# Performance work log

Measured on AMD Instinct MI355X. Metric: run time of the kernel, lower is better.

## Reference

```python
import jax, jax.numpy as jnp
import numpy as np

HEAD_SIZE = 64
N_EMBED = 1024
B, T = 8, 2048


def setup_inputs() -> dict:
    key = jax.random.key(0)
    ks = jax.random.split(key, 7)
    s = lambda fan_in: 1.0 / np.sqrt(fan_in)
    return {
        "x": jax.random.normal(ks[0], (B, T, N_EMBED), dtype=jnp.float32),
        # Linear weights stored as (in, out) so projection is x @ W + b
        "Wk": jax.random.uniform(ks[1], (N_EMBED, HEAD_SIZE), jnp.float32, -s(N_EMBED), s(N_EMBED)),
        "bk": jax.random.uniform(ks[2], (HEAD_SIZE,), jnp.float32, -s(N_EMBED), s(N_EMBED)),
        "Wq": jax.random.uniform(ks[3], (N_EMBED, HEAD_SIZE), jnp.float32, -s(N_EMBED), s(N_EMBED)),
        "bq": jax.random.uniform(ks[4], (HEAD_SIZE,), jnp.float32, -s(N_EMBED), s(N_EMBED)),
        "Wv": jax.random.uniform(ks[5], (N_EMBED, HEAD_SIZE), jnp.float32, -s(N_EMBED), s(N_EMBED)),
        "bv": jax.random.uniform(ks[6], (HEAD_SIZE,), jnp.float32, -s(N_EMBED), s(N_EMBED)),
    }


def reference(x, Wk, bk, Wq, bq, Wv, bv):
    Bb, Tt, C = x.shape
    k = x @ Wk + bk  # [B,T,H]
    q = x @ Wq + bq
    v = x @ Wv + bv
    # NOTE: original computes k @ q^T (keys as rows, queries as cols)
    wei = jnp.einsum("bth,bsh->bts", k, q) * (C ** -0.5)  # [B,T,T]
    causal = jnp.tril(jnp.ones((Tt, Tt), dtype=bool))
    wei = jnp.where(causal, wei, -jnp.inf)
    # softplus instead of softmax; softplus(-inf) = 0, stable via logaddexp
    wei = jnp.logaddexp(wei, 0.0)
    # dropout omitted (eval mode / deterministic reference)
    out = jnp.einsum("bts,bsh->bth", wei, v)  # [B,T,H]
    return out
```

## Files before the change

### kernel.cpp

```cpp
#include <hip/hip_runtime.h>
#include <hip/hip_bf16.h>
#include <stdint.h>

#define HEAD 64
#define CEMB 1024
#define BB 8
#define TSEQ 2048

typedef __attribute__((ext_vector_type(8))) short bf16x8;
typedef __attribute__((ext_vector_type(4))) float f32x4;

__device__ __forceinline__ unsigned short f2bf(float f) {
    union { float f; uint32_t u; } c; c.f = f;
    uint32_t u = c.u + 0x7FFF + ((c.u >> 16) & 1);
    return (unsigned short)(u >> 16);
}
__device__ __forceinline__ ushort4 f4bf(float4 v) {
    ushort4 u; u.x = f2bf(v.x); u.y = f2bf(v.y); u.z = f2bf(v.z); u.w = f2bf(v.w);
    return u;
}

__global__ __launch_bounds__(256) void prep_w(
        const float* __restrict__ Wk, const float* __restrict__ bk,
        const float* __restrict__ Wq, const float* __restrict__ bq,
        const float* __restrict__ Wv, const float* __restrict__ bv,
        unsigned short* __restrict__ WTf, float* __restrict__ biasb) {
    __shared__ float Wl[3][32][64];
    const int kc = blockIdx.x;
    const int tid = threadIdx.x;
    const float* Ws[3] = {Wk, Wq, Wv};
    const int row = tid >> 3, cf = (tid & 7) * 8;
    #pragma unroll
    for (int p = 0; p < 3; p++) {
        const float* W = Ws[p] + (long)(kc * 32 + row) * 64 + cf;
        float4 v0 = *(const float4*)(W);
        float4 v1 = *(const float4*)(W + 4);
        *(float4*)(&Wl[p][row][cf]) = v0;
        *(float4*)(&Wl[p][row][cf + 4]) = v1;
    }
    __syncthreads();
    #pragma unroll
    for (int i = 0; i < 3; i++) {
        int cid = i * 256 + tid;
        int lane = cid & 63;
        int l15 = lane & 15, q4 = lane >> 4;
        int n = (cid >> 6) * 16 + l15;
        int p = n >> 6, col = n & 63;
        float scale = (p == 1) ? 0.03125f : 1.0f;
        unsigned short o[8];
        for (int e = 0; e < 8; e++) o[e] = f2bf(Wl[p][q4 * 8 + e][col] * scale);
        *(int4*)(WTf + (long)kc * 6144 + (long)cid * 8) = *(int4*)o;
    }
    if (kc == 0 && tid < 192) {
        const float* bs[3] = {bk, bq, bv};
        int p = tid >> 6;
        biasb[tid] = bs[p][tid & 63] * ((p == 1) ? 0.03125f : 1.0f);
    }
}

__global__ __launch_bounds__(256) void proj_gemm(
        const float* __restrict__ x, const unsigned short* __restrict__ WTf,
        const float* __restrict__ biasb,
        unsigned short* __restrict__ Kb, unsigned short* __restrict__ Qb,
        unsigned short* __restrict__ VTb) {
    __shared__ __align__(16) unsigned short As[32 * 1032];

    const int tid = threadIdx.x;
    const int lane = tid & 63, w = tid >> 6;
    const int l15 = lane & 15, q4 = lane >> 4;
    const int mw = w & 1, nw = w >> 1;
    const long rowbase = (long)blockIdx.x * 32;

    {
        const int r = tid >> 3, c0 = (tid & 7) * 4;
        const float* xr = x + (rowbase + r) * CEMB + c0;
        float4 buf[32];
        #pragma unroll
        for (int i = 0; i < 32; i++) buf[i] = *(const float4*)(xr + i * 32);
        unsigned short* lr = As + r * 1032 + c0;
        #pragma unroll
        for (int i = 0; i < 32; i++) *(ushort4*)(lr + i * 32) = f4bf(buf[i]);
    }
    __syncthreads();

    f32x4 z = {0.f, 0.f, 0.f, 0.f};
    f32x4 acc[6];
    for (int j = 0; j < 6; j++) acc[j] = z;

    const unsigned short* Am = As + (mw * 16 + l15) * 1032 + q4 * 8;
    const unsigned short* Bg = WTf + (long)(nw * 6) * 512 + (long)lane * 8;

    #pragma unroll 4
    for (int kc = 0; kc < 32; kc++) {
        bf16x8 a = *(const bf16x8*)(Am + kc * 32);
        bf16x8 bfr[6];
        #pragma unroll
        for (int j = 0; j < 6; j++)
            bfr[j] = *(const bf16x8*)(Bg + (long)kc * 6144 + j * 512);
        #pragma unroll
        for (int j = 0; j < 6; j++)
            acc[j] = __builtin_amdgcn_mfma_f32_16x16x32_bf16(a, bfr[j], acc[j], 0, 0, 0);
    }

    for (int j = 0; j < 6; j++) {
        const int n = nw * 96 + j * 16 + l15;
        const float bias = biasb[n];
        const long row0 = rowbase + mw * 16 + q4 * 4;
        if (n < 128) {
            unsigned short* dst = (n < 64) ? (Kb + row0 * HEAD + n)
                                           : (Qb + row0 * HEAD + (n - 64));
            for (int r = 0; r < 4; r++)
                dst[r * HEAD] = f2bf(acc[j][r] + bias);
        } else {
            const int h = n - 128;
            const long b = row0 >> 11; const int t = (int)(row0 & 2047);
            ushort4 pk;
            pk.x = f2bf(acc[j][0] + bias);
            pk.y = f2bf(acc[j][1] + bias);
            pk.z = f2bf(acc[j][2] + bias);
            pk.w = f2bf(acc[j][3] + bias);
            *(ushort4*)(VTb + b * (HEAD * (long)TSEQ) + (long)h * TSEQ + t) = pk;
        }
    }
}

__global__ __launch_bounds__(256) void attn(
        const unsigned short* __restrict__ Kb, const unsigned short* __restrict__ Qb,
        const unsigned short* __restrict__ VTb, float* __restrict__ out) {
    __shared__ __align__(16) unsigned short Pl[4][2][32 * 40];
    __shared__ __align__(16) float red[3][64 * 36];

    const int tid = threadIdx.x;
    const int lane = tid & 63, w = tid >> 6;
    const int l15 = lane & 15, q4 = lane >> 4;

    const int bid = blockIdx.x;
    const int ti = 63 - (bid >> 3);
    const int b = bid & 7;
    const int t0 = ti * 32;

    const unsigned short* kb  = Kb  + (long)b * TSEQ * HEAD;
    const unsigned short* qb  = Qb  + (long)b * TSEQ * HEAD;
    const unsigned short* vtb = VTb + (long)b * HEAD * TSEQ;

    bf16x8 kf[2][2];
    for (int tt = 0; tt < 2; tt++)
        for (int kk = 0; kk < 2; kk++)
            kf[tt][kk] = *(const bf16x8*)(kb + (t0 + tt * 16 + l15) * HEAD + kk * 32 + q4 * 8);

    f32x4 z = {0.f, 0.f, 0.f, 0.f};
    f32x4 oacc[4][2];
    for (int hh = 0; hh < 4; hh++) for (int tt = 0; tt < 2; tt++) oacc[hh][tt] = z;

    bf16x8 qpf[2][2], vpf[4];
    if (w <= ti) {
        const int s0 = w * 32;
        for (int st2 = 0; st2 < 2; st2++)
            for (int kk = 0; kk < 2; kk++)
                qpf[st2][kk] = *(const bf16x8*)(qb + (s0 + st2 * 16 + l15) * HEAD + kk * 32 + q4 * 8);
        for (int hh = 0; hh < 4; hh++)
            vpf[hh] = *(const bf16x8*)(vtb + (hh * 16 + l15) * (long)TSEQ + s0 + q4 * 8);
    }

    int buf = 0;
    for (int c = w; c <= ti; c += 4) {
        const int s0 = c * 32;
        unsigned short* myP = &Pl[w][buf][0];

        bf16x8 qf[2][2], vf[4];
        for (int st2 = 0; st2 < 2; st2++)
            for (int kk = 0; kk < 2; kk++) qf[st2][kk] = qpf[st2][kk];
        for (int hh = 0; hh < 4; hh++) vf[hh] = vpf[hh];

        if (c + 4 <= ti) {
            const int sn = (c + 4) * 32;
            for (int st2 = 0; st2 < 2; st2++)
                for (int kk = 0; kk < 2; kk++)
                    qpf[st2][kk] = *(const bf16x8*)(qb + (sn + st2 * 16 + l15) * HEAD + kk * 32 + q4 * 8);
            for (int hh = 0; hh < 4; hh++)
                vpf[hh] = *(const bf16x8*)(vtb + (hh * 16 + l15) * (long)TSEQ + sn + q4 * 8);
        }

        f32x4 sc[2][2];
        for (int st2 = 0; st2 < 2; st2++)
            for (int tt = 0; tt < 2; tt++) {
                f32x4 s = z;
                s = __builtin_amdgcn_mfma_f32_16x16x32_bf16(qf[st2][0], kf[tt][0], s, 0, 0, 0);
                s = __builtin_amdgcn_mfma_f32_16x16x32_bf16(qf[st2][1], kf[tt][1], s, 0, 0, 0);
                sc[st2][tt] = s;
            }
        for (int tt = 0; tt < 2; tt++) {
            const int tg = t0 + tt * 16 + l15;
            for (int st2 = 0; st2 < 2; st2++) {
                ushort4 pk;
                unsigned short pv[4];
                for (int r = 0; r < 4; r++) {
                    int sg = s0 + st2 * 16 + q4 * 4 + r;
                    float p = __logf(1.0f + __expf(sc[st2][tt][r]));
                    if (sg > tg) p = 0.0f;
                    pv[r] = f2bf(p);
                }
                pk.x = pv[0]; pk.y = pv[1]; pk.z = pv[2]; pk.w = pv[3];
                *(ushort4*)(myP + (tt * 16 + l15) * 40 + st2 * 16 + q4 * 4) = pk;
            }
        }
        __threadfence_block();
        bf16x8 pf0 = *(const bf16x8*)(myP + l15 * 40 + q4 * 8);
        bf16x8 pf1 = *(const bf16x8*)(myP + (16 + l15) * 40 + q4 * 8);
        for (int hh = 0; hh < 4; hh++) {
            oacc[hh][0] = __builtin_amdgcn_mfma_f32_16x16x32_bf16(vf[hh], pf0, oacc[hh][0], 0, 0, 0);
            oacc[hh][1] = __builtin_amdgcn_mfma_f32_16x16x32_bf16(vf[hh], pf1, oacc[hh][1], 0, 0, 0);
        }
        buf ^= 1;
    }

    if (w > 0) {
        float* r0 = &red[w - 1][lane * 36];
        for (int hh = 0; hh < 4; hh++)
            for (int tt = 0; tt < 2; tt++)
                *(f32x4*)(r0 + (hh * 2 + tt) * 4) = oacc[hh][tt];
    }
    __syncthreads();
    if (w == 0) {
        for (int i = 0; i < 3; i++) {
            const float* r0 = &red[i][lane * 36];
            for (int hh = 0; hh < 4; hh++)
                for (int tt = 0; tt < 2; tt++)
                    oacc[hh][tt] += *(const f32x4*)(r0 + (hh * 2 + tt) * 4);
        }
        for (int tt = 0; tt < 2; tt++) {
            float* ob = out + ((long)b * TSEQ + t0 + tt * 16 + l15) * HEAD + q4 * 4;
            for (int hh = 0; hh < 4; hh++)
                *(f32x4*)(ob + hh * 16) = oacc[hh][tt];
        }
    }
}

extern "C" void kernel_launch(void* const* d_in, const int* in_sizes, int n_in,
                              void* d_out, int out_size, void* d_ws, size_t ws_size,
                              hipStream_t stream) {
    const float* x  = (const float*)d_in[0];
    const float* Wk = (const float*)d_in[1];
    const float* bk = (const float*)d_in[2];
    const float* Wq = (const float*)d_in[3];
    const float* bq = (const float*)d_in[4];
    const float* Wv = (const float*)d_in[5];
    const float* bv = (const float*)d_in[6];
    float* out = (float*)d_out;

    char* ws = (char*)d_ws;
    unsigned short* WTf   = (unsigned short*)(ws);
    float*          biasb = (float*)(ws + 393216);
    unsigned short* Kb    = (unsigned short*)(ws + 524288);
    unsigned short* Qb    = (unsigned short*)(ws + 524288 + 2097152);
    unsigned short* VTb   = (unsigned short*)(ws + 524288 + 4194304);

    prep_w<<<32, 256, 0, stream>>>(Wk, bk, Wq, bq, Wv, bv, WTf, biasb);
    proj_gemm<<<512, 256, 0, stream>>>(x, WTf, biasb, Kb, Qb, VTb);
    attn<<<512, 256, 0, stream>>>(Kb, Qb, VTb, out);
}
```

Measured before the change: 153.4 us.

## Restructure projection GEMM with register-resident weights and pipelined x staging

```diff
diff --git a/kernel.cpp b/kernel.cpp
--- a/kernel.cpp
+++ b/kernel.cpp
@@ -58,67 +58,98 @@
     }
 }
 
-__global__ __launch_bounds__(256) void proj_gemm(
+__global__ __launch_bounds__(768) void proj_gemm(
         const float* __restrict__ x, const unsigned short* __restrict__ WTf,
         const float* __restrict__ biasb,
         unsigned short* __restrict__ Kb, unsigned short* __restrict__ Qb,
         unsigned short* __restrict__ VTb) {
-    __shared__ __align__(16) unsigned short As[32 * 1032];
+    __shared__ __align__(16) unsigned short As[64 * 1032];
 
     const int tid = threadIdx.x;
     const int lane = tid & 63, w = tid >> 6;
     const int l15 = lane & 15, q4 = lane >> 4;
-    const int mw = w & 1, nw = w >> 1;
-    const long rowbase = (long)blockIdx.x * 32;
-
+    const long rowbase = (long)blockIdx.x * 64;
+    const float* xg = x + rowbase * CEMB;
+
+    bf16x8 Breg[32];
     {
-        const int r = tid >> 3, c0 = (tid & 7) * 4;
-        const float* xr = x + (rowbase + r) * CEMB + c0;
-        float4 buf[32];
+        const unsigned short* Bg = WTf + w * 512 + (long)lane * 8;
         #pragma unroll
-        for (int i = 0; i < 32; i++) buf[i] = *(const float4*)(xr + i * 32);
-        unsigned short* lr = As + r * 1032 + c0;
+        for (int kc = 0; kc < 32; kc++)
+            Breg[kc] = *(const bf16x8*)(Bg + (long)kc * 6144);
+    }
+
+    f32x4 z = {0.f, 0.f, 0.f, 0.f};
+    f32x4 acc[4];
+    #pragma unroll
+    for (int m = 0; m < 4; m++) acc[m] = z;
+
+    {
         #pragma unroll
-        for (int i = 0; i < 32; i++) *(ushort4*)(lr + i * 32) = f4bf(buf[i]);
+        for (int it = 0; it < 3; it++) {
+            int i = it * 768 + tid;
+            if (i < 2048) {
+                int row = i >> 5, c4 = (i & 31) * 4;
+                float4 v = *(const float4*)(xg + row * CEMB + c4);
+                *(ushort4*)(As + row * 1032 + c4) = f4bf(v);
+            }
+        }
     }
     __syncthreads();
 
-    f32x4 z = {0.f, 0.f, 0.f, 0.f};
-    f32x4 acc[6];
-    for (int j = 0; j < 6; j++) acc[j] = z;
-
-    const unsigned short* Am = As + (mw * 16 + l15) * 1032 + q4 * 8;
-    const unsigned short* Bg = WTf + (long)(nw * 6) * 512 + (long)lane * 8;
-
-    #pragma unroll 4
-    for (int kc = 0; kc < 32; kc++) {
-        bf16x8 a = *(const bf16x8*)(Am + kc * 32);
-        bf16x8 bfr[6];
+    #pragma unroll
+    for (int s = 0; s < 8; s++) {
+        float4 pf[3];
+        if (s < 7) {
+            #pragma unroll
+            for (int it = 0; it < 3; it++) {
+                int i = it * 768 + tid;
+                if (i < 2048) {
+                    int row = i >> 5, c4 = (i & 31) * 4;
+                    pf[it] = *(const float4*)(xg + row * CEMB + (s + 1) * 128 + c4);
+                }
+            }
+        }
         #pragma unroll
-        for (int j = 0; j < 6; j++)
-            bfr[j] = *(const bf16x8*)(Bg + (long)kc * 6144 + j * 512);
-        #pragma unroll
-        for (int j = 0; j < 6; j++)
-            acc[j] = __builtin_amdgcn_mfma_f32_16x16x32_bf16(a, bfr[j], acc[j], 0, 0, 0);
-    }
-
-    for (int j = 0; j < 6; j++) {
-        const int n = nw * 96 + j * 16 + l15;
-        const float bias = biasb[n];
-        const long row0 = rowbase + mw * 16 + q4 * 4;
+        for (int kc = 0; kc < 4; kc++) {
+            const int kg = s * 4 + kc;
+            #pragma unroll
+            for (int m = 0; m < 4; m++) {
+                bf16x8 a = *(const bf16x8*)(As + (m * 16 + l15) * 1032 + kg * 32 + q4 * 8);
+                acc[m] = __builtin_amdgcn_mfma_f32_16x16x32_bf16(a, Breg[kg], acc[m], 0, 0, 0);
+            }
+        }
+        if (s < 7) {
+            #pragma unroll
+            for (int it = 0; it < 3; it++) {
+                int i = it * 768 + tid;
+                if (i < 2048) {
+                    int row = i >> 5, c4 = (i & 31) * 4;
+                    *(ushort4*)(As + row * 1032 + (s + 1) * 128 + c4) = f4bf(pf[it]);
+                }
+            }
+            __syncthreads();
+        }
+    }
+
+    const int n = w * 16 + l15;
+    const float bias = biasb[n];
+    #pragma unroll
+    for (int m = 0; m < 4; m++) {
+        const long row0 = rowbase + m * 16 + q4 * 4;
         if (n < 128) {
             unsigned short* dst = (n < 64) ? (Kb + row0 * HEAD + n)
                                            : (Qb + row0 * HEAD + (n - 64));
             for (int r = 0; r < 4; r++)
-                dst[r * HEAD] = f2bf(acc[j][r] + bias);
+                dst[r * HEAD] = f2bf(acc[m][r] + bias);
         } else {
             const int h = n - 128;
             const long b = row0 >> 11; const int t = (int)(row0 & 2047);
             ushort4 pk;
-            pk.x = f2bf(acc[j][0] + bias);
-            pk.y = f2bf(acc[j][1] + bias);
-            pk.z = f2bf(acc[j][2] + bias);
-            pk.w = f2bf(acc[j][3] + bias);
+            pk.x = f2bf(acc[m][0] + bias);
+            pk.y = f2bf(acc[m][1] + bias);
+            pk.z = f2bf(acc[m][2] + bias);
+            pk.w = f2bf(acc[m][3] + bias);
             *(ushort4*)(VTb + b * (HEAD * (long)TSEQ) + (long)h * TSEQ + t) = pk;
         }
     }
@@ -256,6 +287,6 @@
     unsigned short* VTb   = (unsigned short*)(ws + 524288 + 4194304);
 
     prep_w<<<32, 256, 0, stream>>>(Wk, bk, Wq, bq, Wv, bv, WTf, biasb);
-    proj_gemm<<<512, 256, 0, stream>>>(x, WTf, biasb, Kb, Qb, VTb);
+    proj_gemm<<<256, 768, 0, stream>>>(x, WTf, biasb, Kb, Qb, VTb);
     attn<<<512, 256, 0, stream>>>(Kb, Qb, VTb, out);
 }
```

Measured after the change: 146.0 us. 1.05x faster.
